# Kernel tuning notes

Hardware: AMD Instinct MI355X
Metric: run time of the kernel (lower is better)

The kernel has to match this reference:

```python
import jax, jax.numpy as jnp
import numpy as np

D_MODEL = 256
N_LAYER = 4
D_INNER = 512   # expand=2
D_STATE = 16
DT_RANK = 16    # ceil(d_model/16)
D_CONV = 4
VOCAB = 16
BATCH = 1
SEQLEN = 4096
EPS = 1e-5


def setup_inputs() -> dict:
    key = jax.random.key(0)
    ks = jax.random.split(key, 10)
    s = 0.02
    A_init = jnp.log(jnp.arange(1, D_STATE + 1, dtype=jnp.float32))  # S4D-real init
    return {
        "input_ids": jax.random.randint(ks[0], (BATCH, SEQLEN), 0, VOCAB, dtype=jnp.int32),
        "embed_w": jax.random.normal(ks[1], (VOCAB, D_MODEL), jnp.float32) * s,
        "norm_w": jnp.ones((N_LAYER, D_MODEL), jnp.float32),
        "in_proj_w": jax.random.normal(ks[2], (N_LAYER, 2 * D_INNER, D_MODEL), jnp.float32) * s,
        "out_proj_w": jax.random.normal(ks[3], (N_LAYER, D_MODEL, D_INNER), jnp.float32) * s,
        "conv_w": jax.random.normal(ks[4], (N_LAYER, 2, D_INNER, D_CONV), jnp.float32) * s,
        "conv_b": jnp.zeros((N_LAYER, 2, D_INNER), jnp.float32),
        "x_proj_w": jax.random.normal(ks[5], (N_LAYER, 2, DT_RANK + 2 * D_STATE, D_INNER), jnp.float32) * s,
        "dt_proj_w": jax.random.normal(ks[6], (N_LAYER, 2, D_INNER, DT_RANK), jnp.float32) * s,
        "dt_proj_b": jax.random.normal(ks[7], (N_LAYER, 2, D_INNER), jnp.float32) * 0.1,
        "A_log": jnp.broadcast_to(A_init, (N_LAYER, 2, D_INNER, D_STATE)) + 0.0,
        "Dp": jnp.ones((N_LAYER, 2, D_INNER), jnp.float32),
        "norm_f_w": jnp.ones((D_MODEL,), jnp.float32),
    }


def rmsnorm(x, w):
    return x * jax.lax.rsqrt(jnp.mean(x * x, axis=-1, keepdims=True) + EPS) * w


def selective_scan(u, dt, A, Bm, Cm, Dv):
    # u, dt: (B,L,Di); A: (Di,N); Bm, Cm: (B,L,N); Dv: (Di,)
    dA = jnp.exp(dt[..., None] * A)                         # (B,L,Di,N)
    dBu = dt[..., None] * Bm[:, :, None, :] * u[..., None]  # (B,L,Di,N)

    def step(h, xs):
        dA_t, dBu_t, C_t = xs
        h = dA_t * h + dBu_t                                # (B,Di,N)
        y = jnp.einsum('bdn,bn->bd', h, C_t)
        return h, y

    h0 = jnp.zeros((u.shape[0], D_INNER, D_STATE), u.dtype)
    xs = (jnp.moveaxis(dA, 1, 0), jnp.moveaxis(dBu, 1, 0), jnp.moveaxis(Cm, 1, 0))
    _, ys = jax.lax.scan(step, h0, xs)                      # (L,B,Di)
    return jnp.moveaxis(ys, 0, 1) + u * Dv


def mamba_dir(x, in_w, out_w, cw, cb, xpw, dtw, dtb, a_log, dv):
    # x: (B,L,D)
    xz = jnp.einsum('bld,ed->ble', x, in_w)                 # (B,L,2*Di)
    u, z = jnp.split(xz, 2, axis=-1)
    # causal depthwise conv1d
    uc = jnp.moveaxis(u, 1, 2)                              # (B,Di,L)
    uc = jax.lax.conv_general_dilated(
        uc, cw[:, None, :], (1,), [(D_CONV - 1, 0)],
        feature_group_count=D_INNER, dimension_numbers=('NCH', 'OIH', 'NCH'))
    u = jax.nn.silu(jnp.moveaxis(uc, 1, 2) + cb)            # (B,L,Di)
    xdb = jnp.einsum('bld,ed->ble', u, xpw)                 # (B,L,dt_rank+2N)
    dt_r, Bm, Cm = jnp.split(xdb, [DT_RANK, DT_RANK + D_STATE], axis=-1)
    dt = jax.nn.softplus(jnp.einsum('blr,dr->bld', dt_r, dtw) + dtb)
    A = -jnp.exp(a_log)                                     # (Di,N)
    y = selective_scan(u, dt, A, Bm, Cm, dv)
    y = y * jax.nn.silu(z)
    return jnp.einsum('bld,od->blo', y, out_w)


def reference(input_ids, embed_w, norm_w, in_proj_w, out_proj_w, conv_w, conv_b,
              x_proj_w, dt_proj_w, dt_proj_b, A_log, Dp, norm_f_w):
    h = embed_w[input_ids]                                  # (B,L,D)
    residual = None
    for i in range(N_LAYER):
        residual = h if residual is None else h + residual  # residual_in_fp32
        hn = rmsnorm(residual, norm_w[i])
        out_f = mamba_dir(hn, in_proj_w[i], out_proj_w[i], conv_w[i, 0], conv_b[i, 0],
                          x_proj_w[i, 0], dt_proj_w[i, 0], dt_proj_b[i, 0], A_log[i, 0], Dp[i, 0])
        out_r = mamba_dir(hn[:, ::-1], in_proj_w[i], out_proj_w[i], conv_w[i, 1], conv_b[i, 1],
                          x_proj_w[i, 1], dt_proj_w[i, 1], dt_proj_b[i, 1], A_log[i, 1], Dp[i, 1])[:, ::-1]
        h = out_f + out_r                                   # bidirectional 'add'
    residual = h + residual
    return rmsnorm(residual, norm_f_w)
```

## Files before the change

### kernel.cpp

```cpp
#include <hip/hip_runtime.h>
#include <hip/hip_bf16.h>
#include <math.h>

#define L_  4096
#define D_  256
#define DI_ 512
#define NS_ 16
#define NC_ 128
#define CH_ 32

typedef __attribute__((ext_vector_type(8))) short short8;
typedef __attribute__((ext_vector_type(4))) short short4v;
typedef __attribute__((ext_vector_type(4))) float f32x4;

__global__ __launch_bounds__(256) void embed_kernel(const int* __restrict__ ids,
    const float* __restrict__ ew, float* __restrict__ res) {
  int idx = blockIdx.x * 256 + threadIdx.x;
  int l = idx >> 8, d = idx & 255;
  res[idx] = ew[ids[l] * D_ + d];
}

__global__ __launch_bounds__(256) void convert_weights(const float* __restrict__ inw,
    const float* __restrict__ outw, __hip_bfloat16* __restrict__ inw_b,
    __hip_bfloat16* __restrict__ outw_b) {
  int idx = blockIdx.x * 256 + threadIdx.x;
  inw_b[idx] = __float2bfloat16(inw[idx]);
  int layer = idx >> 18;
  int rem = idx & 262143;
  int o = rem >> 10, k = rem & 1023;
  outw_b[idx] = __float2bfloat16(outw[((size_t)layer * 256 + o) * 512 + (k & 511)]);
}

__global__ __launch_bounds__(256) void convert_xpw(const float* __restrict__ xpw,
    __hip_bfloat16* __restrict__ xpw_b) {
  int idx = blockIdx.x * 256 + threadIdx.x;
  int layer = idx >> 16;
  int rem = idx & 65535;
  int dir = rem >> 15;
  int r = (rem >> 9) & 63, k = idx & 511;
  float v = (r < 48) ? xpw[(((size_t)layer * 2 + dir) * 48 + r) * 512 + k] : 0.f;
  xpw_b[idx] = __float2bfloat16(v);
}

template<bool BF16OUT>
__global__ __launch_bounds__(256) void rmsnorm_kernel(float* __restrict__ residual,
    const float* __restrict__ hadd, const float* __restrict__ w, void* __restrict__ out) {
  int row = blockIdx.x * 4 + (threadIdx.x >> 6);
  int lane = threadIdx.x & 63;
  size_t o = (size_t)row * D_ + lane * 4;
  float4 v = *(const float4*)(residual + o);
  if (hadd) {
    float4 a = *(const float4*)(hadd + o);
    v.x += a.x; v.y += a.y; v.z += a.z; v.w += a.w;
    *(float4*)(residual + o) = v;
  }
  float sq = fmaf(v.x, v.x, fmaf(v.y, v.y, fmaf(v.z, v.z, v.w * v.w)));
  #pragma unroll
  for (int s = 32; s > 0; s >>= 1) sq += __shfl_xor(sq, s, 64);
  float scale = rsqrtf(sq * (1.f / D_) + 1e-5f);
  float4 wv = *(const float4*)(w + lane * 4);
  float r0 = v.x * scale * wv.x, r1 = v.y * scale * wv.y;
  float r2 = v.z * scale * wv.z, r3 = v.w * scale * wv.w;
  if (BF16OUT) {
    __hip_bfloat16* ob = (__hip_bfloat16*)out + o;
    short4v s4;
    s4[0] = __bfloat16_as_short(__float2bfloat16(r0));
    s4[1] = __bfloat16_as_short(__float2bfloat16(r1));
    s4[2] = __bfloat16_as_short(__float2bfloat16(r2));
    s4[3] = __bfloat16_as_short(__float2bfloat16(r3));
    *reinterpret_cast<short4v*>(ob) = s4;
  } else {
    float4 r = {r0, r1, r2, r3};
    *((float4*)out + (o >> 2)) = r;
  }
}

__device__ __forceinline__ void gload_lds16(const void* g, void* l) {
  __builtin_amdgcn_global_load_lds((const __attribute__((address_space(1))) unsigned int*)g,
                                   (__attribute__((address_space(3))) unsigned int*)l,
                                   16, 0, 0);
}

template<int BM, int BN, bool BF16OUT>
__global__ __launch_bounds__(256) void gemm_bt_bf16(const __hip_bfloat16* __restrict__ A,
    const __hip_bfloat16* __restrict__ B, void* __restrict__ Cv, int M, int N, int K,
    size_t sA, size_t sB, size_t sC) {
  A += (size_t)blockIdx.z * sA; B += (size_t)blockIdx.z * sB;
  constexpr int FM = (BM / 2) / 16, FN = (BN / 2) / 16;
  constexpr int ABYTES = BM * 64, BBYTES = BN * 64;
  __shared__ __attribute__((aligned(16))) char As[ABYTES];
  __shared__ __attribute__((aligned(16))) char Bs[BBYTES];
  int tid = threadIdx.x, lane = tid & 63, w = tid >> 6;
  int bm = blockIdx.y * BM, bn = blockIdx.x * BN;
  int wr = (w >> 1) * (BM / 2), wc = (w & 1) * (BN / 2);
  f32x4 acc[FM][FN] = {};
  for (int k0 = 0; k0 < K; k0 += 32) {
    __syncthreads();
    #pragma unroll
    for (int i = 0; i < ABYTES / 4096; ++i) {
      int x = (i * 256 + tid) * 16;
      int xs = x ^ (((x >> 7) & 3) << 4);
      int row = xs >> 6, col = (xs & 63) >> 1;
      gload_lds16(A + (size_t)(bm + row) * K + k0 + col, As + i * 4096 + w * 1024);
    }
    if constexpr (ABYTES % 4096) {
      if (tid < (ABYTES % 4096) / 16) {
        int x = ((ABYTES / 4096) * 256 + tid) * 16;
        int xs = x ^ (((x >> 7) & 3) << 4);
        int row = xs >> 6, col = (xs & 63) >> 1;
        gload_lds16(A + (size_t)(bm + row) * K + k0 + col, As + (ABYTES / 4096) * 4096 + w * 1024);
      }
    }
    #pragma unroll
    for (int i = 0; i < BBYTES / 4096; ++i) {
      int x = (i * 256 + tid) * 16;
      int xs = x ^ (((x >> 7) & 3) << 4);
      int row = xs >> 6, col = (xs & 63) >> 1;
      gload_lds16(B + (size_t)(bn + row) * K + k0 + col, Bs + i * 4096 + w * 1024);
    }
    if constexpr (BBYTES % 4096) {
      if (tid < (BBYTES % 4096) / 16) {
        int x = ((BBYTES / 4096) * 256 + tid) * 16;
        int xs = x ^ (((x >> 7) & 3) << 4);
        int row = xs >> 6, col = (xs & 63) >> 1;
        gload_lds16(B + (size_t)(bn + row) * K + k0 + col, Bs + (BBYTES / 4096) * 4096 + w * 1024);
      }
    }
    __syncthreads();
    short8 af[FM], bf[FN];
    #pragma unroll
    for (int m = 0; m < FM; ++m) {
      int row = wr + m * 16 + (lane & 15);
      int x = row * 64 + ((lane >> 4) * 16);
      x ^= ((x >> 7) & 3) << 4;
      af[m] = *reinterpret_cast<const short8*>(As + x);
    }
    #pragma unroll
    for (int n = 0; n < FN; ++n) {
      int row = wc + n * 16 + (lane & 15);
      int x = row * 64 + ((lane >> 4) * 16);
      x ^= ((x >> 7) & 3) << 4;
      bf[n] = *reinterpret_cast<const short8*>(Bs + x);
    }
    #pragma unroll
    for (int m = 0; m < FM; ++m)
      #pragma unroll
      for (int n = 0; n < FN; ++n)
        acc[m][n] = __builtin_amdgcn_mfma_f32_16x16x32_bf16(af[m], bf[n], acc[m][n], 0, 0, 0);
  }
  #pragma unroll
  for (int m = 0; m < FM; ++m)
    #pragma unroll
    for (int n = 0; n < FN; ++n)
      #pragma unroll
      for (int j = 0; j < 4; ++j) {
        size_t off = (size_t)blockIdx.z * sC +
                     (size_t)(bm + wr + m * 16 + (lane >> 4) * 4 + j) * N + bn + wc + n * 16 + (lane & 15);
        if (BF16OUT) ((__hip_bfloat16*)Cv)[off] = __float2bfloat16(acc[m][n][j]);
        else         ((float*)Cv)[off] = acc[m][n][j];
      }
}

__global__ __launch_bounds__(256) void conv_silu_kernel(const __hip_bfloat16* __restrict__ xz,
    const float* __restrict__ cw, const float* __restrict__ cb,
    __hip_bfloat16* __restrict__ ucb) {
  int dir = blockIdx.y;
  int idx = blockIdx.x * 256 + threadIdx.x;
  int d = idx & (DI_ - 1), l = idx >> 9;
  const float* w = cw + (size_t)dir * DI_ * 4 + (size_t)d * 4;
  float acc = cb[(size_t)dir * DI_ + d];
  #pragma unroll
  for (int k = 0; k < 4; ++k) {
    int lf = l - 3 + k;
    if (lf >= 0) {
      int pos = dir ? (L_ - 1 - lf) : lf;
      acc = fmaf(w[k], __bfloat162float(xz[(size_t)pos * 1024 + d]), acc);
    }
  }
  float s = acc * __builtin_amdgcn_rcpf(1.f + __expf(-acc));
  ucb[(size_t)dir * L_ * DI_ + (size_t)l * DI_ + d] = __float2bfloat16(s);
}

__device__ __forceinline__ void scan_stage(int tid, int lane, int w, int q, int dir,
    const float* __restrict__ xdb, const __hip_bfloat16* __restrict__ uc,
    const float* __restrict__ dtw, const float* __restrict__ dtbp, int c,
    float (*sxdb)[64], unsigned short (*su)[128], float (*sdt)[128]) {
  const char* bg = (const char*)(xdb + ((size_t)dir * L_ + (size_t)c * CH_) * 64);
  const char* ug = (const char*)(uc + ((size_t)dir * L_ + (size_t)c * CH_) * DI_ + q * 128);
  #pragma unroll
  for (int i = 0; i < 2; ++i)
    gload_lds16(bg + w * 2048 + i * 1024 + lane * 16,
                (char*)sxdb + w * 2048 + i * 1024);
  #pragma unroll
  for (int i = 0; i < 2; ++i) {
    int unit = w * 128 + i * 64 + lane;
    int byte = unit * 16;
    gload_lds16(ug + (byte >> 8) * 1024 + (byte & 255),
                (char*)su + w * 2048 + i * 1024);
  }
  __syncthreads();
  int dlx = tid & 127, tst = tid >> 7;
  int dc = q * 128 + dlx;
  const float4* wr = (const float4*)(dtw + ((size_t)dir * DI_ + dc) * 16);
  float4 w0 = wr[0], w1 = wr[1], w2 = wr[2], w3 = wr[3];
  float bias = dtbp[(size_t)dir * DI_ + dc];
  #pragma unroll
  for (int i = 0; i < 16; ++i) {
    int t = tst + i * 2;
    const float4* xr = (const float4*)&sxdb[t][0];
    float4 x0 = xr[0], x1 = xr[1], x2 = xr[2], x3 = xr[3];
    float acc = bias;
    acc = fmaf(w0.x, x0.x, fmaf(w0.y, x0.y, fmaf(w0.z, x0.z, fmaf(w0.w, x0.w, acc))));
    acc = fmaf(w1.x, x1.x, fmaf(w1.y, x1.y, fmaf(w1.z, x1.z, fmaf(w1.w, x1.w, acc))));
    acc = fmaf(w2.x, x2.x, fmaf(w2.y, x2.y, fmaf(w2.z, x2.z, fmaf(w2.w, x2.w, acc))));
    acc = fmaf(w3.x, x3.x, fmaf(w3.y, x3.y, fmaf(w3.z, x3.z, fmaf(w3.w, x3.w, acc))));
    float e = __expf(fminf(acc, 20.f));
    sdt[t][dlx] = acc > 20.f ? acc : __logf(1.f + e);
  }
  __syncthreads();
}

__global__ __launch_bounds__(256) void scan_pass1(const __hip_bfloat16* __restrict__ uc,
    const float* __restrict__ xdb, const float* __restrict__ dtw,
    const float* __restrict__ dtbp, const float* __restrict__ A_log,
    float* __restrict__ Pb, float* __restrict__ Qb) {
  int dir = blockIdx.y;
  int c = blockIdx.x >> 2, q = blockIdx.x & 3;
  int tid = threadIdx.x, lane = tid & 63, w = tid >> 6;
  int dl = tid >> 1, nh = tid & 1;
  int d = q * 128 + dl;
  __shared__ __attribute__((aligned(16))) float sxdb[CH_][64];
  __shared__ __attribute__((aligned(16))) unsigned short su[CH_][128];
  __shared__ __attribute__((aligned(16))) float sdt[CH_][128];
  float Av[8], P[8], Q[8];
  const float4* Ab4 = (const float4*)(A_log + ((size_t)dir * DI_ + d) * 16 + nh * 8);
  float4 a0 = Ab4[0], a1 = Ab4[1];
  float al[8] = {a0.x, a0.y, a0.z, a0.w, a1.x, a1.y, a1.z, a1.w};
  #pragma unroll
  for (int j = 0; j < 8; ++j) { Av[j] = -__expf(al[j]); P[j] = 1.f; Q[j] = 0.f; }
  scan_stage(tid, lane, w, q, dir, xdb, uc, dtw, dtbp, c, sxdb, su, sdt);
  #pragma unroll 2
  for (int t = 0; t < CH_; ++t) {
    float dtv = sdt[t][dl];
    float uv  = __uint_as_float((unsigned)su[t][dl] << 16);
    float du = dtv * uv;
    const float4* Br = (const float4*)&sxdb[t][16 + nh * 8];
    float4 b0 = Br[0], b1 = Br[1];
    float bb[8] = {b0.x, b0.y, b0.z, b0.w, b1.x, b1.y, b1.z, b1.w};
    #pragma unroll
    for (int j = 0; j < 8; ++j) {
      float dA = __expf(dtv * Av[j]);
      P[j] *= dA;
      Q[j] = fmaf(dA, Q[j], bb[j] * du);
    }
  }
  size_t ob = ((size_t)dir * NC_ + c) * 8192 + (size_t)(nh * 8) * 512 + d;
  #pragma unroll
  for (int j = 0; j < 8; ++j) { Pb[ob + j * 512] = P[j]; Qb[ob + j * 512] = Q[j]; }
}

__global__ __launch_bounds__(64) void scan_combine(const float* __restrict__ Pb,
    const float* __restrict__ Qb, float* __restrict__ H0) {
  int idx = blockIdx.x * 64 + threadIdx.x;
  int dir = idx >> 13; int s = idx & 8191;
  size_t base = (size_t)dir * NC_ * 8192 + s;
  float h = 0.f;
  #pragma unroll 8
  for (int c = 0; c < NC_; ++c) {
    size_t o = base + (size_t)c * 8192;
    H0[o] = h;
    h = fmaf(Pb[o], h, Qb[o]);
  }
}

__global__ __launch_bounds__(256) void scan_pass2(const __hip_bfloat16* __restrict__ uc,
    const float* __restrict__ xdb, const float* __restrict__ dtw,
    const float* __restrict__ dtbp, const float* __restrict__ A_log,
    const float* __restrict__ Dp, const __hip_bfloat16* __restrict__ xz,
    const float* __restrict__ H0, __hip_bfloat16* __restrict__ yg) {
  int dir = blockIdx.y;
  int c = blockIdx.x >> 2, q = blockIdx.x & 3;
  int tid = threadIdx.x, lane = tid & 63, w = tid >> 6;
  int dl = tid >> 1, nh = tid & 1;
  int d = q * 128 + dl;
  __shared__ __attribute__((aligned(16))) float sxdb[CH_][64];
  __shared__ __attribute__((aligned(16))) unsigned short su[CH_][128];
  __shared__ __attribute__((aligned(16))) float sdt[CH_][128];
  float Av[8], h[8];
  const float4* Ab4 = (const float4*)(A_log + ((size_t)dir * DI_ + d) * 16 + nh * 8);
  float4 a0 = Ab4[0], a1 = Ab4[1];
  float al[8] = {a0.x, a0.y, a0.z, a0.w, a1.x, a1.y, a1.z, a1.w};
  size_t ob = ((size_t)dir * NC_ + c) * 8192 + (size_t)(nh * 8) * 512 + d;
  #pragma unroll
  for (int j = 0; j < 8; ++j) { Av[j] = -__expf(al[j]); h[j] = H0[ob + j * 512]; }
  float Dv = Dp[(size_t)dir * DI_ + d];
  scan_stage(tid, lane, w, q, dir, xdb, uc, dtw, dtbp, c, sxdb, su, sdt);
  #pragma unroll 2
  for (int t = 0; t < CH_; ++t) {
    float dtv = sdt[t][dl];
    float uv  = __uint_as_float((unsigned)su[t][dl] << 16);
    float du = dtv * uv;
    const float4* Br = (const float4*)&sxdb[t][16 + nh * 8];
    const float4* Cr = (const float4*)&sxdb[t][32 + nh * 8];
    float4 b0 = Br[0], b1 = Br[1], c0 = Cr[0], c1 = Cr[1];
    float bb[8] = {b0.x, b0.y, b0.z, b0.w, b1.x, b1.y, b1.z, b1.w};
    float cc[8] = {c0.x, c0.y, c0.z, c0.w, c1.x, c1.y, c1.z, c1.w};
    float y = 0.f;
    #pragma unroll
    for (int j = 0; j < 8; ++j) {
      float dA = __expf(dtv * Av[j]);
      h[j] = fmaf(dA, h[j], bb[j] * du);
      y = fmaf(h[j], cc[j], y);
    }
    y += __shfl_xor(y, 1, 64);
    if (nh == 0) {
      int l = c * CH_ + t;
      int pos = dir ? (L_ - 1 - l) : l;
      float zv = __bfloat162float(xz[(size_t)pos * 1024 + DI_ + d]);
      float g = zv * __builtin_amdgcn_rcpf(1.f + __expf(-zv));
      yg[(size_t)pos * 1024 + (size_t)dir * DI_ + d] = __float2bfloat16((y + uv * Dv) * g);
    }
  }
}

extern "C" void kernel_launch(void* const* d_in, const int* in_sizes, int n_in,
                              void* d_out, int out_size, void* d_ws, size_t ws_size,
                              hipStream_t stream) {
  const int*   ids       = (const int*)  d_in[0];
  const float* embed_w   = (const float*)d_in[1];
  const float* norm_w    = (const float*)d_in[2];
  const float* in_proj_w = (const float*)d_in[3];
  const float* out_proj_w= (const float*)d_in[4];
  const float* conv_w    = (const float*)d_in[5];
  const float* conv_b    = (const float*)d_in[6];
  const float* x_proj_w  = (const float*)d_in[7];
  const float* dt_proj_w = (const float*)d_in[8];
  const float* dt_proj_b = (const float*)d_in[9];
  const float* A_log     = (const float*)d_in[10];
  const float* Dp        = (const float*)d_in[11];
  const float* norm_f_w  = (const float*)d_in[12];

  float* ws = (float*)d_ws;
  float* residual = ws; ws += (size_t)L_ * D_;
  float* xdb      = ws; ws += (size_t)2 * L_ * 64;
  float* hbuf     = ws; ws += (size_t)L_ * D_;
  float* Pb       = ws; ws += (size_t)2 * NC_ * 8192;
  float* Qb       = ws; ws += (size_t)2 * NC_ * 8192;
  float* H0       = ws; ws += (size_t)2 * NC_ * 8192;
  __hip_bfloat16* hn_b   = (__hip_bfloat16*)ws;
  __hip_bfloat16* xz_b   = hn_b + (size_t)L_ * D_;
  __hip_bfloat16* yg_b   = xz_b + (size_t)L_ * 1024;
  __hip_bfloat16* uc_b   = yg_b + (size_t)L_ * 1024;
  __hip_bfloat16* inw_b  = uc_b + (size_t)2 * L_ * DI_;
  __hip_bfloat16* outw_b = inw_b + (size_t)4 * 1024 * D_;
  __hip_bfloat16* xpw_b  = outw_b + (size_t)4 * D_ * 1024;

  embed_kernel<<<L_ * D_ / 256, 256, 0, stream>>>(ids, embed_w, residual);
  convert_weights<<<4 * 1024 * D_ / 256, 256, 0, stream>>>(in_proj_w, out_proj_w, inw_b, outw_b);
  convert_xpw<<<4 * 2 * 64 * 512 / 256, 256, 0, stream>>>(x_proj_w, xpw_b);

  for (int i = 0; i < 4; ++i) {
    rmsnorm_kernel<true><<<L_ / 4, 256, 0, stream>>>(residual, i ? hbuf : nullptr,
                                                     norm_w + (size_t)i * D_, hn_b);
    gemm_bt_bf16<128, 64, true><<<dim3(1024 / 64, L_ / 128, 1), 256, 0, stream>>>(
        hn_b, inw_b + (size_t)i * 1024 * D_, xz_b, L_, 1024, D_, 0, 0, 0);
    dim3 gdi(L_ * DI_ / 256, 2);
    conv_silu_kernel<<<gdi, 256, 0, stream>>>(
        xz_b, conv_w + (size_t)i * 2 * DI_ * 4, conv_b + (size_t)i * 2 * DI_, uc_b);
    gemm_bt_bf16<32, 64, false><<<dim3(1, L_ / 32, 2), 256, 0, stream>>>(
        uc_b, xpw_b + (size_t)i * 2 * 64 * DI_, xdb, L_, 64, DI_,
        (size_t)L_ * DI_, (size_t)64 * DI_, (size_t)L_ * 64);
    dim3 gsc(NC_ * 4, 2);
    scan_pass1<<<gsc, 256, 0, stream>>>(
        uc_b, xdb, dt_proj_w + (size_t)i * 2 * DI_ * 16, dt_proj_b + (size_t)i * 2 * DI_,
        A_log + (size_t)i * 2 * DI_ * NS_, Pb, Qb);
    scan_combine<<<256, 64, 0, stream>>>(Pb, Qb, H0);
    scan_pass2<<<gsc, 256, 0, stream>>>(
        uc_b, xdb, dt_proj_w + (size_t)i * 2 * DI_ * 16, dt_proj_b + (size_t)i * 2 * DI_,
        A_log + (size_t)i * 2 * DI_ * NS_, Dp + (size_t)i * 2 * DI_,
        xz_b, H0, yg_b);
    gemm_bt_bf16<64, 64, false><<<dim3(D_ / 64, L_ / 64, 1), 256, 0, stream>>>(
        yg_b, outw_b + (size_t)i * D_ * 1024, hbuf, L_, D_, 1024, 0, 0, 0);
  }

  rmsnorm_kernel<false><<<L_ / 4, 256, 0, stream>>>(residual, hbuf, norm_f_w, d_out);
}
```

Baseline: 485.0 us.

## Split out-proj per direction, vectorize conv, merge prep kernels, retile in-proj

Merges the embedding and three weight-conversion launches into one prep kernel and stops duplicating out_proj weights. The out-projection becomes a batched GEMM over the two directions with K=512 instead of one GEMM with K=1024. Its two partial outputs are summed inside the next rmsnorm. The conv+SiLU kernel now processes 8 channels per thread with 16-byte loads and stores, and the in-proj GEMM tile shrinks from 128 to 64 rows to launch more blocks. In exchange there is an extra fp32 buffer read per rmsnorm and a different yg layout.

Measured after the change: 509.2 us. 1.05x slower.

```diff
diff --git a/kernel.cpp b/kernel.cpp
--- a/kernel.cpp
+++ b/kernel.cpp
@@ -13,45 +13,39 @@
 typedef __attribute__((ext_vector_type(4))) short short4v;
 typedef __attribute__((ext_vector_type(4))) float f32x4;
 
-__global__ __launch_bounds__(256) void embed_kernel(const int* __restrict__ ids,
-    const float* __restrict__ ew, float* __restrict__ res) {
+__global__ __launch_bounds__(256) void prep_kernel(const int* __restrict__ ids,
+    const float* __restrict__ ew, const float* __restrict__ inw,
+    const float* __restrict__ outw, const float* __restrict__ xpw,
+    float* __restrict__ res, __hip_bfloat16* __restrict__ inw_b,
+    __hip_bfloat16* __restrict__ outw_b, __hip_bfloat16* __restrict__ xpw_b) {
   int idx = blockIdx.x * 256 + threadIdx.x;
   int l = idx >> 8, d = idx & 255;
   res[idx] = ew[ids[l] * D_ + d];
-}
-
-__global__ __launch_bounds__(256) void convert_weights(const float* __restrict__ inw,
-    const float* __restrict__ outw, __hip_bfloat16* __restrict__ inw_b,
-    __hip_bfloat16* __restrict__ outw_b) {
-  int idx = blockIdx.x * 256 + threadIdx.x;
   inw_b[idx] = __float2bfloat16(inw[idx]);
-  int layer = idx >> 18;
-  int rem = idx & 262143;
-  int o = rem >> 10, k = rem & 1023;
-  outw_b[idx] = __float2bfloat16(outw[((size_t)layer * 256 + o) * 512 + (k & 511)]);
-}
-
-__global__ __launch_bounds__(256) void convert_xpw(const float* __restrict__ xpw,
-    __hip_bfloat16* __restrict__ xpw_b) {
-  int idx = blockIdx.x * 256 + threadIdx.x;
-  int layer = idx >> 16;
-  int rem = idx & 65535;
-  int dir = rem >> 15;
-  int r = (rem >> 9) & 63, k = idx & 511;
-  float v = (r < 48) ? xpw[(((size_t)layer * 2 + dir) * 48 + r) * 512 + k] : 0.f;
-  xpw_b[idx] = __float2bfloat16(v);
+  if (idx < 4 * 256 * 512)
+    outw_b[idx] = __float2bfloat16(outw[idx]);
+  if (idx < 4 * 2 * 64 * 512) {
+    int layer = idx >> 16;
+    int rem = idx & 65535;
+    int dir = rem >> 15;
+    int r = (rem >> 9) & 63, k = idx & 511;
+    float v = (r < 48) ? xpw[(((size_t)layer * 2 + dir) * 48 + r) * 512 + k] : 0.f;
+    xpw_b[idx] = __float2bfloat16(v);
+  }
 }
 
 template<bool BF16OUT>
 __global__ __launch_bounds__(256) void rmsnorm_kernel(float* __restrict__ residual,
-    const float* __restrict__ hadd, const float* __restrict__ w, void* __restrict__ out) {
+    const float* __restrict__ h0, const float* __restrict__ h1,
+    const float* __restrict__ w, void* __restrict__ out) {
   int row = blockIdx.x * 4 + (threadIdx.x >> 6);
   int lane = threadIdx.x & 63;
   size_t o = (size_t)row * D_ + lane * 4;
   float4 v = *(const float4*)(residual + o);
-  if (hadd) {
-    float4 a = *(const float4*)(hadd + o);
-    v.x += a.x; v.y += a.y; v.z += a.z; v.w += a.w;
+  if (h0) {
+    float4 a = *(const float4*)(h0 + o);
+    float4 b = *(const float4*)(h1 + o);
+    v.x += a.x + b.x; v.y += a.y + b.y; v.z += a.z + b.z; v.w += a.w + b.w;
     *(float4*)(residual + o) = v;
   }
   float sq = fmaf(v.x, v.x, fmaf(v.y, v.y, fmaf(v.z, v.z, v.w * v.w)));
@@ -165,20 +159,32 @@
     const float* __restrict__ cw, const float* __restrict__ cb,
     __hip_bfloat16* __restrict__ ucb) {
   int dir = blockIdx.y;
-  int idx = blockIdx.x * 256 + threadIdx.x;
-  int d = idx & (DI_ - 1), l = idx >> 9;
-  const float* w = cw + (size_t)dir * DI_ * 4 + (size_t)d * 4;
-  float acc = cb[(size_t)dir * DI_ + d];
+  int i8 = blockIdx.x * 256 + threadIdx.x;
+  int l = i8 >> 6, d0 = (i8 & 63) * 8;
+  const float* wp = cw + ((size_t)dir * DI_ + d0) * 4;
+  float acc[8];
+  #pragma unroll
+  for (int j = 0; j < 8; ++j) acc[j] = cb[(size_t)dir * DI_ + d0 + j];
   #pragma unroll
   for (int k = 0; k < 4; ++k) {
     int lf = l - 3 + k;
     if (lf >= 0) {
       int pos = dir ? (L_ - 1 - lf) : lf;
-      acc = fmaf(w[k], __bfloat162float(xz[(size_t)pos * 1024 + d]), acc);
-    }
-  }
-  float s = acc * __builtin_amdgcn_rcpf(1.f + __expf(-acc));
-  ucb[(size_t)dir * L_ * DI_ + (size_t)l * DI_ + d] = __float2bfloat16(s);
+      short8 xv = *reinterpret_cast<const short8*>(xz + (size_t)pos * 1024 + d0);
+      #pragma unroll
+      for (int j = 0; j < 8; ++j) {
+        float xf = __uint_as_float((unsigned)(unsigned short)xv[j] << 16);
+        acc[j] = fmaf(wp[j * 4 + k], xf, acc[j]);
+      }
+    }
+  }
+  short8 o8;
+  #pragma unroll
+  for (int j = 0; j < 8; ++j) {
+    float s = acc[j] * __builtin_amdgcn_rcpf(1.f + __expf(-acc[j]));
+    o8[j] = __bfloat16_as_short(__float2bfloat16(s));
+  }
+  *reinterpret_cast<short8*>(ucb + ((size_t)dir * L_ + l) * DI_ + d0) = o8;
 }
 
 __device__ __forceinline__ void scan_stage(int tid, int lane, int w, int q, int dir,
@@ -318,7 +324,7 @@
       int pos = dir ? (L_ - 1 - l) : l;
       float zv = __bfloat162float(xz[(size_t)pos * 1024 + DI_ + d]);
       float g = zv * __builtin_amdgcn_rcpf(1.f + __expf(-zv));
-      yg[(size_t)pos * 1024 + (size_t)dir * DI_ + d] = __float2bfloat16((y + uv * Dv) * g);
+      yg[((size_t)dir * L_ + pos) * DI_ + d] = __float2bfloat16((y + uv * Dv) * g);
     }
   }
 }
@@ -343,29 +349,28 @@
   float* ws = (float*)d_ws;
   float* residual = ws; ws += (size_t)L_ * D_;
   float* xdb      = ws; ws += (size_t)2 * L_ * 64;
-  float* hbuf     = ws; ws += (size_t)L_ * D_;
+  float* hbuf2    = ws; ws += (size_t)2 * L_ * D_;
   float* Pb       = ws; ws += (size_t)2 * NC_ * 8192;
   float* Qb       = ws; ws += (size_t)2 * NC_ * 8192;
   float* H0       = ws; ws += (size_t)2 * NC_ * 8192;
   __hip_bfloat16* hn_b   = (__hip_bfloat16*)ws;
   __hip_bfloat16* xz_b   = hn_b + (size_t)L_ * D_;
   __hip_bfloat16* yg_b   = xz_b + (size_t)L_ * 1024;
-  __hip_bfloat16* uc_b   = yg_b + (size_t)L_ * 1024;
+  __hip_bfloat16* uc_b   = yg_b + (size_t)2 * L_ * DI_;
   __hip_bfloat16* inw_b  = uc_b + (size_t)2 * L_ * DI_;
   __hip_bfloat16* outw_b = inw_b + (size_t)4 * 1024 * D_;
-  __hip_bfloat16* xpw_b  = outw_b + (size_t)4 * D_ * 1024;
-
-  embed_kernel<<<L_ * D_ / 256, 256, 0, stream>>>(ids, embed_w, residual);
-  convert_weights<<<4 * 1024 * D_ / 256, 256, 0, stream>>>(in_proj_w, out_proj_w, inw_b, outw_b);
-  convert_xpw<<<4 * 2 * 64 * 512 / 256, 256, 0, stream>>>(x_proj_w, xpw_b);
+  __hip_bfloat16* xpw_b  = outw_b + (size_t)4 * D_ * DI_;
+
+  prep_kernel<<<L_ * D_ / 256, 256, 0, stream>>>(ids, embed_w, in_proj_w, out_proj_w,
+                                                 x_proj_w, residual, inw_b, outw_b, xpw_b);
 
   for (int i = 0; i < 4; ++i) {
-    rmsnorm_kernel<true><<<L_ / 4, 256, 0, stream>>>(residual, i ? hbuf : nullptr,
-                                                     norm_w + (size_t)i * D_, hn_b);
-    gemm_bt_bf16<128, 64, true><<<dim3(1024 / 64, L_ / 128, 1), 256, 0, stream>>>(
+    rmsnorm_kernel<true><<<L_ / 4, 256, 0, stream>>>(
+        residual, i ? hbuf2 : nullptr, i ? hbuf2 + (size_t)L_ * D_ : nullptr,
+        norm_w + (size_t)i * D_, hn_b);
+    gemm_bt_bf16<64, 64, true><<<dim3(1024 / 64, L_ / 64, 1), 256, 0, stream>>>(
         hn_b, inw_b + (size_t)i * 1024 * D_, xz_b, L_, 1024, D_, 0, 0, 0);
-    dim3 gdi(L_ * DI_ / 256, 2);
-    conv_silu_kernel<<<gdi, 256, 0, stream>>>(
+    conv_silu_kernel<<<dim3(L_ * DI_ / 8 / 256, 2), 256, 0, stream>>>(
         xz_b, conv_w + (size_t)i * 2 * DI_ * 4, conv_b + (size_t)i * 2 * DI_, uc_b);
     gemm_bt_bf16<32, 64, false><<<dim3(1, L_ / 32, 2), 256, 0, stream>>>(
         uc_b, xpw_b + (size_t)i * 2 * 64 * DI_, xdb, L_, 64, DI_,
@@ -379,9 +384,11 @@
         uc_b, xdb, dt_proj_w + (size_t)i * 2 * DI_ * 16, dt_proj_b + (size_t)i * 2 * DI_,
         A_log + (size_t)i * 2 * DI_ * NS_, Dp + (size_t)i * 2 * DI_,
         xz_b, H0, yg_b);
-    gemm_bt_bf16<64, 64, false><<<dim3(D_ / 64, L_ / 64, 1), 256, 0, stream>>>(
-        yg_b, outw_b + (size_t)i * D_ * 1024, hbuf, L_, D_, 1024, 0, 0, 0);
-  }
-
-  rmsnorm_kernel<false><<<L_ / 4, 256, 0, stream>>>(residual, hbuf, norm_f_w, d_out);
-}
+    gemm_bt_bf16<64, 64, false><<<dim3(D_ / 64, L_ / 64, 2), 256, 0, stream>>>(
+        yg_b, outw_b + (size_t)i * D_ * DI_, hbuf2, L_, D_, DI_,
+        (size_t)L_ * DI_, 0, (size_t)L_ * D_);
+  }
+
+  rmsnorm_kernel<false><<<L_ / 4, 256, 0, stream>>>(
+      residual, hbuf2, hbuf2 + (size_t)L_ * D_, norm_f_w, d_out);
+}
```
